# Kernel optimization log

Measured on AMD Instinct MI355X. Metric: run time of the kernel, lower is better.

The kernel has to match this reference:

```python
import jax, jax.numpy as jnp
import numpy as np

VOCAB = 30000
EMB = 128
ENC = 128
BS = 256
DEPTH = 10            # perfect binary tree depth
N = 2 ** DEPTH - 1    # 1023 nodes per tree, heap layout: children of i are 2i+1, 2i+2


def setup_inputs() -> dict:
    key = jax.random.key(0)
    k1, k2, k3, k4 = jax.random.split(key, 4)
    tokens = jax.random.randint(k1, (BS, N), 0, VOCAB)                       # node token ids
    emb = jax.random.normal(k2, (VOCAB, EMB), jnp.float32) * 0.02            # embedding table
    W_c = jax.random.normal(k3, (ENC, EMB), jnp.float32) / np.sqrt(EMB)      # Linear weight [out,in]
    b_c = jax.random.normal(k4, (ENC,), jnp.float32) * 0.01                  # Linear bias
    return {"tokens": tokens, "emb": emb, "W_c": W_c, "b_c": b_c, "bs": BS}


def reference(tokens, emb, W_c, b_c, bs):
    # Per-node leaf contribution: c = W_c(embedding(token))  -> [bs, N, ENC]
    c = jnp.einsum('bne,oe->bno', emb[tokens], W_c) + b_c
    # Bottom-up tree sum: h[i] = c[i] + h[2i+1] + h[2i+2]
    h = c
    for l in reversed(range(DEPTH - 1)):          # fixed small loop over tree depth
        s = 2 ** l - 1
        e = 2 ** (l + 1) - 1
        left = h[:, 2 * s + 1:2 * e:2]            # children of parents [s, e)
        right = h[:, 2 * s + 2:2 * e + 1:2]
        h = h.at[:, s:e].add(left + right)
    # Max-pool over all nodes of each tree (original: max over stacked node_list)
    return jnp.max(h, axis=1)                     # [bs, ENC]
```

## Files before the change

kernel.cpp:

```cpp
#include <hip/hip_runtime.h>
#include <hip/hip_bf16.h>
#include <stdint.h>

#define VOCAB 30000
#define EMB 128
#define ENC 128
#define BS 256
#define NNODES 1023

typedef short short8 __attribute__((ext_vector_type(8)));
typedef float f32x4 __attribute__((ext_vector_type(4)));

__device__ __forceinline__ unsigned short f2bf(float x) {
    uint32_t u = __float_as_uint(x);
    uint32_t r = u + 0x7fffu + ((u >> 16) & 1u);
    return (unsigned short)(r >> 16);
}
__device__ __forceinline__ float bf2f(unsigned short h) {
    return __uint_as_float(((uint32_t)h) << 16);
}

#define WLD 136
__global__ void __launch_bounds__(256) project_k(const float* __restrict__ emb,
                                                 const float* __restrict__ W,
                                                 const float* __restrict__ bias,
                                                 unsigned short* __restrict__ P) {
    __shared__ unsigned short Wlds[ENC * WLD];

    for (int i = threadIdx.x; i < ENC * EMB; i += 256) {
        const int o = i >> 7, k = i & 127;
        Wlds[o * WLD + k] = f2bf(W[i]);
    }
    __syncthreads();

    const int wave = threadIdx.x >> 6;
    const int lane = threadIdx.x & 63;
    const int r = lane & 15;
    const int q = lane >> 4;
    const int v0 = blockIdx.x * 64 + wave * 16;

    int vr = v0 + r;
    if (vr > VOCAB - 1) vr = VOCAB - 1;

    short8 af[4];
    const float* erow = emb + (size_t)vr * EMB + q * 8;
#pragma unroll
    for (int kk = 0; kk < 4; kk++) {
        const float4 x0 = *(const float4*)(erow + kk * 32);
        const float4 x1 = *(const float4*)(erow + kk * 32 + 4);
        short8 a;
        a[0] = (short)f2bf(x0.x); a[1] = (short)f2bf(x0.y);
        a[2] = (short)f2bf(x0.z); a[3] = (short)f2bf(x0.w);
        a[4] = (short)f2bf(x1.x); a[5] = (short)f2bf(x1.y);
        a[6] = (short)f2bf(x1.z); a[7] = (short)f2bf(x1.w);
        af[kk] = a;
    }

#pragma unroll
    for (int ot = 0; ot < 8; ot++) {
        const int o0 = ot * 16;
        f32x4 acc = {0.f, 0.f, 0.f, 0.f};
        const unsigned short* wrow = Wlds + (o0 + r) * WLD + q * 8;
#pragma unroll
        for (int kk = 0; kk < 4; kk++) {
            short8 bf = *(const short8*)(wrow + kk * 32);
            acc = __builtin_amdgcn_mfma_f32_16x16x32_bf16(af[kk], bf, acc, 0, 0, 0);
        }
        const float bb = bias[o0 + r];
#pragma unroll
        for (int i = 0; i < 4; i++) {
            const int vo = v0 + q * 4 + i;
            if (vo < VOCAB) P[(size_t)vo * ENC + o0 + r] = f2bf(acc[i] + bb);
        }
    }
}

__global__ void __launch_bounds__(256) subtree_k(const int* __restrict__ tokens,
                                                 const unsigned short* __restrict__ P,
                                                 float* __restrict__ sums,
                                                 float* __restrict__ maxes) {
    const int lane = threadIdx.x & 63;
    const int w    = threadIdx.x >> 6;
    const int b    = blockIdx.y;
    const int st   = blockIdx.x * 4 + w;
    const int* tb  = tokens + b * NNODES;
    const int rp1  = 32 + st;
    const uint32_t* Pw = (const uint32_t*)P;

    float2 m2; m2.x = -3.0e38f; m2.y = -3.0e38f;
    float2 v[16];
    int base = (rp1 << 4) - 1;
#pragma unroll
    for (int i = 0; i < 16; i++) {
        const uint32_t p = Pw[(size_t)tb[base + i] * 64 + lane];
        v[i].x = __uint_as_float(p << 16);
        v[i].y = __uint_as_float(p & 0xffff0000u);
    }
#pragma unroll
    for (int i = 0; i < 16; i++) { m2.x = fmaxf(m2.x, v[i].x); m2.y = fmaxf(m2.y, v[i].y); }

    float2 u[8];
    base = (rp1 << 3) - 1;
#pragma unroll
    for (int i = 0; i < 8; i++) {
        const uint32_t p = Pw[(size_t)tb[base + i] * 64 + lane];
        u[i].x = __uint_as_float(p << 16)         + v[2 * i].x + v[2 * i + 1].x;
        u[i].y = __uint_as_float(p & 0xffff0000u) + v[2 * i].y + v[2 * i + 1].y;
        m2.x = fmaxf(m2.x, u[i].x); m2.y = fmaxf(m2.y, u[i].y);
    }
    float2 w4[4];
    base = (rp1 << 2) - 1;
#pragma unroll
    for (int i = 0; i < 4; i++) {
        const uint32_t p = Pw[(size_t)tb[base + i] * 64 + lane];
        w4[i].x = __uint_as_float(p << 16)         + u[2 * i].x + u[2 * i + 1].x;
        w4[i].y = __uint_as_float(p & 0xffff0000u) + u[2 * i].y + u[2 * i + 1].y;
        m2.x = fmaxf(m2.x, w4[i].x); m2.y = fmaxf(m2.y, w4[i].y);
    }
    float2 w2[2];
    base = (rp1 << 1) - 1;
#pragma unroll
    for (int i = 0; i < 2; i++) {
        const uint32_t p = Pw[(size_t)tb[base + i] * 64 + lane];
        w2[i].x = __uint_as_float(p << 16)         + w4[2 * i].x + w4[2 * i + 1].x;
        w2[i].y = __uint_as_float(p & 0xffff0000u) + w4[2 * i].y + w4[2 * i + 1].y;
        m2.x = fmaxf(m2.x, w2[i].x); m2.y = fmaxf(m2.y, w2[i].y);
    }
    const uint32_t p = Pw[(size_t)tb[rp1 - 1] * 64 + lane];
    float2 s;
    s.x = __uint_as_float(p << 16)         + w2[0].x + w2[1].x;
    s.y = __uint_as_float(p & 0xffff0000u) + w2[0].y + w2[1].y;
    m2.x = fmaxf(m2.x, s.x); m2.y = fmaxf(m2.y, s.y);

    ((float2*)(sums  + (b * 32 + st) * ENC))[lane] = s;
    ((float2*)(maxes + (b * 32 + st) * ENC))[lane] = m2;
}

__global__ void __launch_bounds__(128) topfold_k(const int* __restrict__ tokens,
                                                 const unsigned short* __restrict__ P,
                                                 const float* __restrict__ sums,
                                                 const float* __restrict__ maxes,
                                                 float* __restrict__ out) {
    const int b = blockIdx.x;
    const int ch = threadIdx.x;
    const int* tb = tokens + b * NNODES;

    float m = -3.0e38f;
    float v[32];
#pragma unroll
    for (int i = 0; i < 32; i++) v[i] = sums[(b * 32 + i) * ENC + ch];
#pragma unroll
    for (int i = 0; i < 32; i++) m = fmaxf(m, maxes[(b * 32 + i) * ENC + ch]);

    float u[16];
#pragma unroll
    for (int i = 0; i < 16; i++) {
        u[i] = bf2f(P[(size_t)tb[15 + i] * ENC + ch]) + v[2 * i] + v[2 * i + 1];
        m = fmaxf(m, u[i]);
    }
    float w8[8];
#pragma unroll
    for (int i = 0; i < 8; i++) {
        w8[i] = bf2f(P[(size_t)tb[7 + i] * ENC + ch]) + u[2 * i] + u[2 * i + 1];
        m = fmaxf(m, w8[i]);
    }
    float w4[4];
#pragma unroll
    for (int i = 0; i < 4; i++) {
        w4[i] = bf2f(P[(size_t)tb[3 + i] * ENC + ch]) + w8[2 * i] + w8[2 * i + 1];
        m = fmaxf(m, w4[i]);
    }
    float w2[2];
#pragma unroll
    for (int i = 0; i < 2; i++) {
        w2[i] = bf2f(P[(size_t)tb[1 + i] * ENC + ch]) + w4[2 * i] + w4[2 * i + 1];
        m = fmaxf(m, w2[i]);
    }
    const float s0 = bf2f(P[(size_t)tb[0] * ENC + ch]) + w2[0] + w2[1];
    m = fmaxf(m, s0);

    out[b * ENC + ch] = m;
}

extern "C" void kernel_launch(void* const* d_in, const int* in_sizes, int n_in,
                              void* d_out, int out_size, void* d_ws, size_t ws_size,
                              hipStream_t stream) {
    const int*   tokens = (const int*)d_in[0];
    const float* emb    = (const float*)d_in[1];
    const float* W_c    = (const float*)d_in[2];
    const float* b_c    = (const float*)d_in[3];
    float* out = (float*)d_out;

    char* ws = (char*)d_ws;
    unsigned short* P     = (unsigned short*)ws;
    float*          sums  = (float*)(ws + 7680000);
    float*          maxes = sums + BS * 32 * ENC;

    project_k<<<(VOCAB + 63) / 64, 256, 0, stream>>>(emb, W_c, b_c, P);
    subtree_k<<<dim3(8, BS), 256, 0, stream>>>(tokens, P, sums, maxes);
    topfold_k<<<BS, 128, 0, stream>>>(tokens, P, sums, maxes, out);
}
```

Baseline: 94.34 us.

## Fuse subtree and top-fold kernels into one per-tree block using LDS

Merges the subtree and top-fold kernels into a single kernel with one 512-thread block per tree. Each wave now processes four subtrees, two at a time and interleaved, to expose more independent gathers. Partial sums and maxes are kept in shared memory rather than written to global scratch, which removes one launch and a global round trip. The weight staging in the projection kernel is also vectorised to float4 loads. In exchange the grid drops from 2048 to 256 blocks, the two live subtree states raise register pressure, and the top fold runs on only 128 of 512 threads.

```diff
diff --git a/kernel.cpp b/kernel.cpp
--- a/kernel.cpp
+++ b/kernel.cpp
@@ -27,9 +27,13 @@
                                                  unsigned short* __restrict__ P) {
     __shared__ unsigned short Wlds[ENC * WLD];
 
-    for (int i = threadIdx.x; i < ENC * EMB; i += 256) {
-        const int o = i >> 7, k = i & 127;
-        Wlds[o * WLD + k] = f2bf(W[i]);
+    for (int i = threadIdx.x; i < (ENC * EMB) / 4; i += 256) {
+        const int e = i * 4;
+        const int o = e >> 7, k = e & 127;
+        const float4 x = *(const float4*)(W + e);
+        ushort4 s;
+        s.x = f2bf(x.x); s.y = f2bf(x.y); s.z = f2bf(x.z); s.w = f2bf(x.w);
+        *(ushort4*)(Wlds + o * WLD + k) = s;
     }
     __syncthreads();
 
@@ -75,93 +79,127 @@
     }
 }
 
-__global__ void __launch_bounds__(256) subtree_k(const int* __restrict__ tokens,
-                                                 const unsigned short* __restrict__ P,
-                                                 float* __restrict__ sums,
-                                                 float* __restrict__ maxes) {
+__global__ void __launch_bounds__(512) tree_k(const int* __restrict__ tokens,
+                                              const unsigned short* __restrict__ P,
+                                              float* __restrict__ out) {
+    __shared__ float s_sum[32][ENC];
+    __shared__ float s_max[32][ENC];
+
+    const int b    = blockIdx.x;
     const int lane = threadIdx.x & 63;
     const int w    = threadIdx.x >> 6;
-    const int b    = blockIdx.y;
-    const int st   = blockIdx.x * 4 + w;
     const int* tb  = tokens + b * NNODES;
-    const int rp1  = 32 + st;
     const uint32_t* Pw = (const uint32_t*)P;
 
-    float2 m2; m2.x = -3.0e38f; m2.y = -3.0e38f;
-    float2 v[16];
-    int base = (rp1 << 4) - 1;
+#pragma unroll
+    for (int pr = 0; pr < 2; pr++) {
+        const int st0 = w * 4 + pr * 2;
+        const int st1 = st0 + 1;
+        const int ra = 32 + st0;
+        const int rb = 32 + st1;
+
+        float2 mA, mB;
+        mA.x = mA.y = mB.x = mB.y = -3.0e38f;
+
+        float2 vA[16], vB[16];
+        {
+            const int ba = (ra << 4) - 1, bb_ = (rb << 4) - 1;
+#pragma unroll
+            for (int i = 0; i < 16; i++) {
+                const uint32_t pa = Pw[(size_t)tb[ba + i] * 64 + lane];
+                const uint32_t pb = Pw[(size_t)tb[bb_ + i] * 64 + lane];
+                vA[i].x = __uint_as_float(pa << 16); vA[i].y = __uint_as_float(pa & 0xffff0000u);
+                vB[i].x = __uint_as_float(pb << 16); vB[i].y = __uint_as_float(pb & 0xffff0000u);
+            }
+#pragma unroll
+            for (int i = 0; i < 16; i++) {
+                mA.x = fmaxf(mA.x, vA[i].x); mA.y = fmaxf(mA.y, vA[i].y);
+                mB.x = fmaxf(mB.x, vB[i].x); mB.y = fmaxf(mB.y, vB[i].y);
+            }
+        }
+        float2 uA[8], uB[8];
+        {
+            const int ba = (ra << 3) - 1, bb_ = (rb << 3) - 1;
+#pragma unroll
+            for (int i = 0; i < 8; i++) {
+                const uint32_t pa = Pw[(size_t)tb[ba + i] * 64 + lane];
+                const uint32_t pb = Pw[(size_t)tb[bb_ + i] * 64 + lane];
+                uA[i].x = __uint_as_float(pa << 16)         + vA[2*i].x + vA[2*i+1].x;
+                uA[i].y = __uint_as_float(pa & 0xffff0000u) + vA[2*i].y + vA[2*i+1].y;
+                uB[i].x = __uint_as_float(pb << 16)         + vB[2*i].x + vB[2*i+1].x;
+                uB[i].y = __uint_as_float(pb & 0xffff0000u) + vB[2*i].y + vB[2*i+1].y;
+                mA.x = fmaxf(mA.x, uA[i].x); mA.y = fmaxf(mA.y, uA[i].y);
+                mB.x = fmaxf(mB.x, uB[i].x); mB.y = fmaxf(mB.y, uB[i].y);
+            }
+        }
+        float2 wA[4], wB[4];
+        {
+            const int ba = (ra << 2) - 1, bb_ = (rb << 2) - 1;
+#pragma unroll
+            for (int i = 0; i < 4; i++) {
+                const uint32_t pa = Pw[(size_t)tb[ba + i] * 64 + lane];
+                const uint32_t pb = Pw[(size_t)tb[bb_ + i] * 64 + lane];
+                wA[i].x = __uint_as_float(pa << 16)         + uA[2*i].x + uA[2*i+1].x;
+                wA[i].y = __uint_as_float(pa & 0xffff0000u) + uA[2*i].y + uA[2*i+1].y;
+                wB[i].x = __uint_as_float(pb << 16)         + uB[2*i].x + uB[2*i+1].x;
+                wB[i].y = __uint_as_float(pb & 0xffff0000u) + uB[2*i].y + uB[2*i+1].y;
+                mA.x = fmaxf(mA.x, wA[i].x); mA.y = fmaxf(mA.y, wA[i].y);
+                mB.x = fmaxf(mB.x, wB[i].x); mB.y = fmaxf(mB.y, wB[i].y);
+            }
+        }
+        float2 zA[2], zB[2];
+        {
+            const int ba = (ra << 1) - 1, bb_ = (rb << 1) - 1;
+#pragma unroll
+            for (int i = 0; i < 2; i++) {
+                const uint32_t pa = Pw[(size_t)tb[ba + i] * 64 + lane];
+                const uint32_t pb = Pw[(size_t)tb[bb_ + i] * 64 + lane];
+                zA[i].x = __uint_as_float(pa << 16)         + wA[2*i].x + wA[2*i+1].x;
+                zA[i].y = __uint_as_float(pa & 0xffff0000u) + wA[2*i].y + wA[2*i+1].y;
+                zB[i].x = __uint_as_float(pb << 16)         + wB[2*i].x + wB[2*i+1].x;
+                zB[i].y = __uint_as_float(pb & 0xffff0000u) + wB[2*i].y + wB[2*i+1].y;
+                mA.x = fmaxf(mA.x, zA[i].x); mA.y = fmaxf(mA.y, zA[i].y);
+                mB.x = fmaxf(mB.x, zB[i].x); mB.y = fmaxf(mB.y, zB[i].y);
+            }
+        }
+        {
+            const uint32_t pa = Pw[(size_t)tb[ra - 1] * 64 + lane];
+            const uint32_t pb = Pw[(size_t)tb[rb - 1] * 64 + lane];
+            float2 sA, sB;
+            sA.x = __uint_as_float(pa << 16)         + zA[0].x + zA[1].x;
+            sA.y = __uint_as_float(pa & 0xffff0000u) + zA[0].y + zA[1].y;
+            sB.x = __uint_as_float(pb << 16)         + zB[0].x + zB[1].x;
+            sB.y = __uint_as_float(pb & 0xffff0000u) + zB[0].y + zB[1].y;
+            mA.x = fmaxf(mA.x, sA.x); mA.y = fmaxf(mA.y, sA.y);
+            mB.x = fmaxf(mB.x, sB.x); mB.y = fmaxf(mB.y, sB.y);
+            ((float2*)s_sum[st0])[lane] = sA;
+            ((float2*)s_max[st0])[lane] = mA;
+            ((float2*)s_sum[st1])[lane] = sB;
+            ((float2*)s_max[st1])[lane] = mB;
+        }
+    }
+
+    __syncthreads();
+    if (threadIdx.x >= ENC) return;
+    const int ch = threadIdx.x;
+
+    float m = -3.0e38f;
+    float vv[32];
+#pragma unroll
+    for (int i = 0; i < 32; i++) vv[i] = s_sum[i][ch];
+#pragma unroll
+    for (int i = 0; i < 32; i++) m = fmaxf(m, s_max[i][ch]);
+
+    float uu[16];
 #pragma unroll
     for (int i = 0; i < 16; i++) {
-        const uint32_t p = Pw[(size_t)tb[base + i] * 64 + lane];
-        v[i].x = __uint_as_float(p << 16);
-        v[i].y = __uint_as_float(p & 0xffff0000u);
-    }
-#pragma unroll
-    for (int i = 0; i < 16; i++) { m2.x = fmaxf(m2.x, v[i].x); m2.y = fmaxf(m2.y, v[i].y); }
-
-    float2 u[8];
-    base = (rp1 << 3) - 1;
+        uu[i] = bf2f(P[(size_t)tb[15 + i] * ENC + ch]) + vv[2 * i] + vv[2 * i + 1];
+        m = fmaxf(m, uu[i]);
+    }
+    float w8[8];
 #pragma unroll
     for (int i = 0; i < 8; i++) {
-        const uint32_t p = Pw[(size_t)tb[base + i] * 64 + lane];
-        u[i].x = __uint_as_float(p << 16)         + v[2 * i].x + v[2 * i + 1].x;
-        u[i].y = __uint_as_float(p & 0xffff0000u) + v[2 * i].y + v[2 * i + 1].y;
-        m2.x = fmaxf(m2.x, u[i].x); m2.y = fmaxf(m2.y, u[i].y);
-    }
-    float2 w4[4];
-    base = (rp1 << 2) - 1;
-#pragma unroll
-    for (int i = 0; i < 4; i++) {
-        const uint32_t p = Pw[(size_t)tb[base + i] * 64 + lane];
-        w4[i].x = __uint_as_float(p << 16)         + u[2 * i].x + u[2 * i + 1].x;
-        w4[i].y = __uint_as_float(p & 0xffff0000u) + u[2 * i].y + u[2 * i + 1].y;
-        m2.x = fmaxf(m2.x, w4[i].x); m2.y = fmaxf(m2.y, w4[i].y);
-    }
-    float2 w2[2];
-    base = (rp1 << 1) - 1;
-#pragma unroll
-    for (int i = 0; i < 2; i++) {
-        const uint32_t p = Pw[(size_t)tb[base + i] * 64 + lane];
-        w2[i].x = __uint_as_float(p << 16)         + w4[2 * i].x + w4[2 * i + 1].x;
-        w2[i].y = __uint_as_float(p & 0xffff0000u) + w4[2 * i].y + w4[2 * i + 1].y;
-        m2.x = fmaxf(m2.x, w2[i].x); m2.y = fmaxf(m2.y, w2[i].y);
-    }
-    const uint32_t p = Pw[(size_t)tb[rp1 - 1] * 64 + lane];
-    float2 s;
-    s.x = __uint_as_float(p << 16)         + w2[0].x + w2[1].x;
-    s.y = __uint_as_float(p & 0xffff0000u) + w2[0].y + w2[1].y;
-    m2.x = fmaxf(m2.x, s.x); m2.y = fmaxf(m2.y, s.y);
-
-    ((float2*)(sums  + (b * 32 + st) * ENC))[lane] = s;
-    ((float2*)(maxes + (b * 32 + st) * ENC))[lane] = m2;
-}
-
-__global__ void __launch_bounds__(128) topfold_k(const int* __restrict__ tokens,
-                                                 const unsigned short* __restrict__ P,
-                                                 const float* __restrict__ sums,
-                                                 const float* __restrict__ maxes,
-                                                 float* __restrict__ out) {
-    const int b = blockIdx.x;
-    const int ch = threadIdx.x;
-    const int* tb = tokens + b * NNODES;
-
-    float m = -3.0e38f;
-    float v[32];
-#pragma unroll
-    for (int i = 0; i < 32; i++) v[i] = sums[(b * 32 + i) * ENC + ch];
-#pragma unroll
-    for (int i = 0; i < 32; i++) m = fmaxf(m, maxes[(b * 32 + i) * ENC + ch]);
-
-    float u[16];
-#pragma unroll
-    for (int i = 0; i < 16; i++) {
-        u[i] = bf2f(P[(size_t)tb[15 + i] * ENC + ch]) + v[2 * i] + v[2 * i + 1];
-        m = fmaxf(m, u[i]);
-    }
-    float w8[8];
-#pragma unroll
-    for (int i = 0; i < 8; i++) {
-        w8[i] = bf2f(P[(size_t)tb[7 + i] * ENC + ch]) + u[2 * i] + u[2 * i + 1];
+        w8[i] = bf2f(P[(size_t)tb[7 + i] * ENC + ch]) + uu[2 * i] + uu[2 * i + 1];
         m = fmaxf(m, w8[i]);
     }
     float w4[4];
@@ -191,12 +229,8 @@
     const float* b_c    = (const float*)d_in[3];
     float* out = (float*)d_out;
 
-    char* ws = (char*)d_ws;
-    unsigned short* P     = (unsigned short*)ws;
-    float*          sums  = (float*)(ws + 7680000);
-    float*          maxes = sums + BS * 32 * ENC;
+    unsigned short* P = (unsigned short*)d_ws;
 
     project_k<<<(VOCAB + 63) / 64, 256, 0, stream>>>(emb, W_c, b_c, P);
-    subtree_k<<<dim3(8, BS), 256, 0, stream>>>(tokens, P, sums, maxes);
-    topfold_k<<<BS, 128, 0, stream>>>(tokens, P, sums, maxes, out);
-}
+    tree_k<<<BS, 512, 0, stream>>>(tokens, P, out);
+}
```

Result: faster. 91.68 us (-2.8%).
